# Kernel optimization log

Measured on AMD Instinct MI355X. Metric: run time of the kernel, lower is better.

Reference implementation:

```python
import jax, jax.numpy as jnp
import numpy as np

HEADS = 4
DIM_HEAD = 32
DIM = 128
HIDDEN = HEADS * DIM_HEAD  # 128


def setup_inputs() -> dict:
    key = jax.random.key(0)
    k1, k2, k3, k4 = jax.random.split(key, 4)
    B, C, H, W = 8, DIM, 128, 128
    x = jax.random.normal(k1, (B, C, H, W), dtype=jnp.float32)
    # 1x1 conv weights stored as [out_ch, in_ch] (kernel dims squeezed)
    w_qkv = jax.random.normal(k2, (3 * HIDDEN, DIM), dtype=jnp.float32) * (1.0 / np.sqrt(DIM))
    w_out = jax.random.normal(k3, (DIM, HIDDEN), dtype=jnp.float32) * (1.0 / np.sqrt(HIDDEN))
    b_out = jax.random.normal(k4, (DIM,), dtype=jnp.float32) * 0.01
    return {"x": x, "w_qkv": w_qkv, "w_out": w_out, "b_out": b_out}


def reference(x, w_qkv, w_out, b_out):
    b, c, h, w = x.shape
    n = h * w
    # 1x1 conv == per-pixel matmul over channels
    qkv = jnp.einsum('bchw,oc->bohw', x, w_qkv)            # [b, 3*HIDDEN, h, w]
    # channel layout: (qkv, heads, dim_head)
    qkv = qkv.reshape(b, 3, HEADS, DIM_HEAD, n)            # [b, 3, H, d, n]
    q, k, v = qkv[:, 0], qkv[:, 1], qkv[:, 2]
    k = jax.nn.softmax(k, axis=-1)                         # softmax over spatial n
    context = jnp.einsum('bhdn,bhen->bhde', k, v)          # [b, H, d, d] (tiny)
    out = jnp.einsum('bhde,bhdn->bhen', context, q)        # [b, H, d, n]
    out = out.reshape(b, HIDDEN, h, w)
    y = jnp.einsum('bchw,oc->bohw', out, w_out) + b_out[None, :, None, None]
    return y
```

## Files before the change

### kernel.cpp

```cpp
#include <hip/hip_runtime.h>
#include <math.h>

#define C_ 128
#define N_ 16384

#define WS_Z    0
#define WS_CTX  1024
#define WS_A    164864
#define WS_PCTX 295936
#define WS_PZ   (WS_PCTX + 512*4096)
#define WS_END  (WS_PZ + 512*128)

typedef __attribute__((ext_vector_type(8))) short bf16x8;
typedef __attribute__((ext_vector_type(4))) float f32x4;
typedef __attribute__((ext_vector_type(4))) unsigned int u32x4;
typedef __attribute__((ext_vector_type(2))) unsigned int u32x2;

__device__ __forceinline__ unsigned int pkbf(float a, float b) {
  unsigned int r;
  asm("v_cvt_pk_bf16_f32 %0, %1, %2" : "=v"(r) : "v"(a), "v"(b));
  return r;
}

__device__ __forceinline__ bf16x8 make_frag(float4 u, float4 v) {
  u32x4 q = {pkbf(u.x, u.y), pkbf(u.z, u.w), pkbf(v.x, v.y), pkbf(v.z, v.w)};
  return *(bf16x8*)&q;
}

__device__ __forceinline__ bf16x8 lds_frag16(const unsigned short* p) {
  u32x4 q = *(const u32x4*)p;
  return *(bf16x8*)&q;
}

__device__ __forceinline__ void load4(const float* p, float* o) {
  float4 v = *(const float4*)p;
  o[0] = v.x; o[1] = v.y; o[2] = v.z; o[3] = v.w;
}

__device__ __forceinline__ void* xsa(void* base, int row, int col_bytes) {
  return (void*)((char*)base + row * 272 + (col_bytes ^ (((row >> 4) & 3) << 4)));
}

template<bool ATOMIC>
__global__ __launch_bounds__(512, 2) void k1_kv_ctx(const float* __restrict__ x,
                                                    const float* __restrict__ wqkv,
                                                    float* __restrict__ ws) {
  __shared__ __attribute__((aligned(16))) unsigned short xs[64][136];
  __shared__ __attribute__((aligned(16))) unsigned short ekv[2][128][72];
  const int tid  = threadIdx.x;
  const int wave = tid >> 6;
  const int l15  = tid & 15;
  const int l4   = (tid >> 4) & 3;
  const int b    = blockIdx.y;
  const int j    = blockIdx.x;
  const int h    = wave & 3;
  const int t    = wave >> 2;
  const int kvrow0 = h * 32 + t * 128;
  const float* xb = x + (size_t)b * ((size_t)C_ * N_);

  const int sn4 = tid & 15;
  const int scq = tid >> 4;

  bf16x8 wf[2][4];
  #pragma unroll
  for (int mi = 0; mi < 2; ++mi)
    #pragma unroll
    for (int ki = 0; ki < 4; ++ki) {
      const float* p = wqkv + (size_t)(128 + kvrow0 + mi * 16 + l15) * C_ + ki * 32 + l4 * 8;
      wf[mi][ki] = make_frag(*(const float4*)p, *(const float4*)(p + 4));
    }

  {
    float va[4][4];
    #pragma unroll
    for (int r = 0; r < 4; ++r)
      load4(xb + (size_t)(scq * 4 + r) * N_ + j * 256 + sn4 * 4, va[r]);
    #pragma unroll
    for (int i = 0; i < 4; ++i) {
      u32x2 w = {pkbf(va[0][i], va[1][i]), pkbf(va[2][i], va[3][i])};
      *(u32x2*)xsa(xs, sn4 * 4 + i, scq * 8) = w;
    }
  }
  __syncthreads();

  const f32x4 z4 = {0.f, 0.f, 0.f, 0.f};
  f32x4 ctxacc[2][2];
  #pragma unroll
  for (int i = 0; i < 2; ++i)
    #pragma unroll
    for (int jj = 0; jj < 2; ++jj) ctxacc[i][jj] = z4;
  float zacc[2] = {0.f, 0.f};

  for (int st = 0; st < 4; ++st) {
    float pf[4][4];
    if (st < 3) {
      const int nbn = j * 256 + (st + 1) * 64;
      #pragma unroll
      for (int r = 0; r < 4; ++r)
        load4(xb + (size_t)(scq * 4 + r) * N_ + nbn + sn4 * 4, pf[r]);
    }

    #pragma unroll
    for (int half = 0; half < 2; ++half) {
      f32x4 acc[2][2];
      #pragma unroll
      for (int a = 0; a < 2; ++a)
        #pragma unroll
        for (int m = 0; m < 2; ++m) acc[a][m] = z4;
      #pragma unroll
      for (int ki = 0; ki < 4; ++ki) {
        bf16x8 bfr[2];
        #pragma unroll
        for (int ni2 = 0; ni2 < 2; ++ni2)
          bfr[ni2] = lds_frag16((const unsigned short*)
              xsa(xs, half * 32 + ni2 * 16 + l15, ki * 64 + l4 * 16));
        __builtin_amdgcn_s_setprio(1);
        #pragma unroll
        for (int ni2 = 0; ni2 < 2; ++ni2)
          #pragma unroll
          for (int mi = 0; mi < 2; ++mi)
            acc[ni2][mi] = __builtin_amdgcn_mfma_f32_16x16x32_bf16(
                bfr[ni2], wf[mi][ki], acc[ni2][mi], 0, 0, 0);
        __builtin_amdgcn_s_setprio(0);
      }
      #pragma unroll
      for (int ni2 = 0; ni2 < 2; ++ni2)
        #pragma unroll
        for (int mi = 0; mi < 2; ++mi) {
          float e0, e1, e2, e3;
          if (t == 0) {
            e0 = __expf(acc[ni2][mi][0]); e1 = __expf(acc[ni2][mi][1]);
            e2 = __expf(acc[ni2][mi][2]); e3 = __expf(acc[ni2][mi][3]);
            zacc[mi] += (e0 + e1) + (e2 + e3);
          } else {
            e0 = acc[ni2][mi][0]; e1 = acc[ni2][mi][1];
            e2 = acc[ni2][mi][2]; e3 = acc[ni2][mi][3];
          }
          u32x2 w = {pkbf(e0, e1), pkbf(e2, e3)};
          *(u32x2*)&ekv[t][h * 32 + mi * 16 + l15][(half * 2 + ni2) * 16 + l4 * 4] = w;
        }
    }
    __syncthreads();

    {
      bf16x8 af2[2], bv2[2];
      #pragma unroll
      for (int m2 = 0; m2 < 2; ++m2)
        af2[m2] = lds_frag16(&ekv[0][h * 32 + m2 * 16 + l15][t * 32 + l4 * 8]);
      #pragma unroll
      for (int n2 = 0; n2 < 2; ++n2)
        bv2[n2] = lds_frag16(&ekv[1][h * 32 + n2 * 16 + l15][t * 32 + l4 * 8]);
      __builtin_amdgcn_s_setprio(1);
      #pragma unroll
      for (int m2 = 0; m2 < 2; ++m2)
        #pragma unroll
        for (int n2 = 0; n2 < 2; ++n2)
          ctxacc[m2][n2] = __builtin_amdgcn_mfma_f32_16x16x32_bf16(
              af2[m2], bv2[n2], ctxacc[m2][n2], 0, 0, 0);
      __builtin_amdgcn_s_setprio(0);
    }

    if (st < 3) {
      #pragma unroll
      for (int i = 0; i < 4; ++i) {
        u32x2 w = {pkbf(pf[0][i], pf[1][i]), pkbf(pf[2][i], pf[3][i])};
        *(u32x2*)xsa(xs, sn4 * 4 + i, scq * 8) = w;
      }
    }
    __syncthreads();
  }

  {
    float* csh = (float*)ekv;
    if (t == 1) {
      #pragma unroll
      for (int m2 = 0; m2 < 2; ++m2)
        #pragma unroll
        for (int n2 = 0; n2 < 2; ++n2)
          #pragma unroll
          for (int r = 0; r < 4; ++r)
            csh[h * 1152 + (m2 * 16 + l4 * 4 + r) * 36 + n2 * 16 + l15] =
                ctxacc[m2][n2][r];
    }
    __syncthreads();
    if (t == 0) {
      #pragma unroll
      for (int m2 = 0; m2 < 2; ++m2)
        #pragma unroll
        for (int n2 = 0; n2 < 2; ++n2)
          #pragma unroll
          for (int r = 0; r < 4; ++r)
            ctxacc[m2][n2][r] +=
                csh[h * 1152 + (m2 * 16 + l4 * 4 + r) * 36 + n2 * 16 + l15];
      if (!ATOMIC) {
        float* ps = ws + WS_PCTX + (size_t)(b * 64 + j) * 4096 + h * 1024;
        #pragma unroll
        for (int m2 = 0; m2 < 2; ++m2)
          #pragma unroll
          for (int n2 = 0; n2 < 2; ++n2)
            #pragma unroll
            for (int r = 0; r < 4; ++r)
              ps[(m2 * 16 + l4 * 4 + r) * 32 + n2 * 16 + l15] = ctxacc[m2][n2][r];
      } else {
        float* ctx = ws + WS_CTX + (size_t)(b * 4 + h) * 1024;
        #pragma unroll
        for (int m2 = 0; m2 < 2; ++m2)
          #pragma unroll
          for (int n2 = 0; n2 < 2; ++n2)
            #pragma unroll
            for (int r = 0; r < 4; ++r)
              atomicAdd(&ctx[(m2 * 16 + l4 * 4 + r) * 32 + n2 * 16 + l15],
                        ctxacc[m2][n2][r]);
      }
      #pragma unroll
      for (int mi = 0; mi < 2; ++mi) {
        float z = zacc[mi];
        z += __shfl_xor(z, 16);
        z += __shfl_xor(z, 32);
        if ((tid & 48) == 0) {
          int row = h * 32 + mi * 16 + l15;
          if (!ATOMIC)
            ws[WS_PZ + (size_t)(b * 64 + j) * 128 + row] = z;
          else
            atomicAdd(&ws[WS_Z + b * 128 + row], z);
        }
      }
    }
  }
}

__global__ __launch_bounds__(256) void k1c(float* __restrict__ ws) {
  __shared__ float4 part[4][64];
  const int tid = threadIdx.x;
  const int eq = blockIdx.x;
  const int h  = blockIdx.y;
  const int b  = blockIdx.z;
  const int f4 = tid & 63;
  const int p  = tid >> 6;

  const float* base = ws + WS_PCTX + (size_t)(b * 64) * 4096
                         + h * 1024 + eq * 256 + f4 * 4;
  float4 s = {0.f, 0.f, 0.f, 0.f};
  #pragma unroll 8
  for (int q = 0; q < 16; ++q) {
    float4 v = *(const float4*)(base + (size_t)(p * 16 + q) * 4096);
    s.x += v.x; s.y += v.y; s.z += v.z; s.w += v.w;
  }
  part[p][f4] = s;

  if (eq == 0 && tid < 32) {
    const float* pz = ws + WS_PZ + (size_t)(b * 64) * 128 + h * 32 + tid;
    float z = 0.f;
    #pragma unroll 8
    for (int q = 0; q < 64; ++q) z += pz[(size_t)q * 128];
    ws[WS_Z + b * 128 + h * 32 + tid] = z;
  }
  __syncthreads();

  if (tid < 64) {
    float4 a = part[0][tid], c = part[1][tid], d = part[2][tid], e = part[3][tid];
    float4 o;
    o.x = (a.x + c.x) + (d.x + e.x);
    o.y = (a.y + c.y) + (d.y + e.y);
    o.z = (a.z + c.z) + (d.z + e.z);
    o.w = (a.w + c.w) + (d.w + e.w);
    *(float4*)(ws + WS_CTX + (size_t)(b * 4 + h) * 1024 + eq * 256 + tid * 4) = o;
  }
}

__global__ __launch_bounds__(256) void k2(const float* __restrict__ w_qkv,
                                          const float* __restrict__ w_out,
                                          float* __restrict__ ws) {
  __shared__ float bs[128][132];
  __shared__ float wqs[32][128];
  __shared__ float wos[32][132];
  __shared__ float cn[32][33];
  const int tid = threadIdx.x;
  const int oq = blockIdx.x, b = blockIdx.y;

  for (int h = 0; h < 4; ++h) {
    if (h) __syncthreads();
    const float* Z   = ws + WS_Z + b * 128 + h * 32;
    const float* ctx = ws + WS_CTX + ((b * 4 + h) * 32) * 32;
    #pragma unroll
    for (int k = 0; k < 4; ++k) {
      int idx = tid + k * 256;
      int d = idx >> 5, e = idx & 31;
      cn[d][e] = ctx[d * 32 + e] / Z[d];
    }
    #pragma unroll
    for (int k = 0; k < 4; ++k) {
      int idx = tid + k * 256;
      int d = idx >> 5, f4 = idx & 31;
      *(float4*)&wqs[d][f4 * 4] = *(const float4*)(w_qkv + (h * 32 + d) * 128 + f4 * 4);
    }
    __syncthreads();
    const int e = tid >> 3, cs = (tid & 7) * 16;
    float s[16];
    #pragma unroll
    for (int jj = 0; jj < 16; ++jj) s[jj] = 0.f;
    for (int d = 0; d < 32; ++d) {
      float v = cn[d][e];
      #pragma unroll
      for (int jj = 0; jj < 16; ++jj) s[jj] = fmaf(v, wqs[d][cs + jj], s[jj]);
    }
    #pragma unroll
    for (int jj = 0; jj < 16; ++jj) bs[h * 32 + e][cs + jj] = s[jj];
  }

  __syncthreads();
  #pragma unroll
  for (int k = 0; k < 4; ++k) {
    int idx = tid + k * 256;
    int r = idx >> 5, f4 = idx & 31;
    *(float4*)&wos[r][f4 * 4] = *(const float4*)(w_out + (oq * 32 + r) * 128 + f4 * 4);
  }
  __syncthreads();
  const int ol = tid >> 3, cq = (tid & 7) * 16;
  float s[16];
  #pragma unroll
  for (int jj = 0; jj < 16; ++jj) s[jj] = 0.f;
  for (int eg = 0; eg < 128; ++eg) {
    float w = wos[ol][eg];
    #pragma unroll
    for (int jj = 0; jj < 16; ++jj) s[jj] = fmaf(w, bs[eg][cq + jj], s[jj]);
  }
  float* A = ws + WS_A + ((size_t)b * 128 + oq * 32 + ol) * 128;
  #pragma unroll
  for (int jj = 0; jj < 16; ++jj) A[cq + jj] = s[jj];
}

__global__ __launch_bounds__(512, 2) void k3(const float* __restrict__ x,
                                             const float* __restrict__ bout,
                                             const float* __restrict__ ws,
                                             float* __restrict__ y) {
  __shared__ __attribute__((aligned(16))) unsigned short xs2[2][64][136];
  const int tid  = threadIdx.x;
  const int wave = tid >> 6;
  const int l15  = tid & 15;
  const int l4   = (tid >> 4) & 3;
  const int b    = blockIdx.y;
  const int n0   = blockIdx.x * 256;
  const float* xb = x + (size_t)b * ((size_t)C_ * N_);
  const float* A  = ws + WS_A + (size_t)b * 128 * 128;

  const int sn4 = tid & 15;
  const int scq = tid >> 4;

  bf16x8 af[4];
  #pragma unroll
  for (int ki = 0; ki < 4; ++ki) {
    const float* p = A + (size_t)(wave * 16 + l15) * 128 + ki * 32 + l4 * 8;
    af[ki] = make_frag(*(const float4*)p, *(const float4*)(p + 4));
  }
  const float bias = bout[wave * 16 + l15];

  {
    float va[4][4];
    #pragma unroll
    for (int r = 0; r < 4; ++r)
      load4(xb + (size_t)(scq * 4 + r) * N_ + n0 + sn4 * 4, va[r]);
    #pragma unroll
    for (int i = 0; i < 4; ++i) {
      u32x2 w = {pkbf(va[0][i], va[1][i]), pkbf(va[2][i], va[3][i])};
      *(u32x2*)xsa(&xs2[0][0][0], sn4 * 4 + i, scq * 8) = w;
    }
  }
  __syncthreads();

  const f32x4 z4 = {0.f, 0.f, 0.f, 0.f};
  float* yb = y + (size_t)b * ((size_t)128 * N_);

  for (int st = 0; st < 4; ++st) {
    const int nb = n0 + st * 64;

    float pf[4][4];
    if (st < 3) {
      #pragma unroll
      for (int r = 0; r < 4; ++r)
        load4(xb + (size_t)(scq * 4 + r) * N_ + nb + 64 + sn4 * 4, pf[r]);
    }

    f32x4 acc[4];
    #pragma unroll
    for (int ni = 0; ni < 4; ++ni) acc[ni] = z4;
    #pragma unroll
    for (int ki = 0; ki < 4; ++ki) {
      bf16x8 bfr[4];
      #pragma unroll
      for (int ni = 0; ni < 4; ++ni)
        bfr[ni] = lds_frag16((const unsigned short*)
            xsa(&xs2[st & 1][0][0], ni * 16 + l15, ki * 64 + l4 * 16));
      #pragma unroll
      for (int ni = 0; ni < 4; ++ni)
        acc[ni] = __builtin_amdgcn_mfma_f32_16x16x32_bf16(
            bfr[ni], af[ki], acc[ni], 0, 0, 0);
    }

    if (st < 3) {
      #pragma unroll
      for (int i = 0; i < 4; ++i) {
        u32x2 w = {pkbf(pf[0][i], pf[1][i]), pkbf(pf[2][i], pf[3][i])};
        *(u32x2*)xsa(&xs2[(st + 1) & 1][0][0], sn4 * 4 + i, scq * 8) = w;
      }
    }

    #pragma unroll
    for (int ni = 0; ni < 4; ++ni) {
      float4 o;
      o.x = acc[ni][0] + bias;
      o.y = acc[ni][1] + bias;
      o.z = acc[ni][2] + bias;
      o.w = acc[ni][3] + bias;
      *(float4*)(yb + (size_t)(wave * 16 + l15) * N_ + nb + ni * 16 + l4 * 4) = o;
    }

    if (st < 3) __syncthreads();
  }
}

extern "C" void kernel_launch(void* const* d_in, const int* in_sizes, int n_in,
                              void* d_out, int out_size, void* d_ws, size_t ws_size,
                              hipStream_t stream) {
  const float* x     = (const float*)d_in[0];
  const float* w_qkv = (const float*)d_in[1];
  const float* w_out = (const float*)d_in[2];
  const float* b_out = (const float*)d_in[3];
  float* y  = (float*)d_out;
  float* ws = (float*)d_ws;

  const bool partial = ws_size >= (size_t)WS_END * sizeof(float);
  if (partial) {
    k1_kv_ctx<false><<<dim3(64, 8), 512, 0, stream>>>(x, w_qkv, ws);
    k1c<<<dim3(4, 4, 8), 256, 0, stream>>>(ws);
  } else {
    hipMemsetAsync(ws, 0, (1024 + 32768) * sizeof(float), stream);
    k1_kv_ctx<true><<<dim3(64, 8), 512, 0, stream>>>(x, w_qkv, ws);
  }
  k2<<<dim3(4, 8), 256, 0, stream>>>(w_qkv, w_out, ws);
  k3<<<dim3(64, 8), 512, 0, stream>>>(x, b_out, ws, y);
}
```

Measured before the change: 73.16 us.

## Fuse all stages into one cooperative persistent kernel with grid syncs

Merges the context-projection, partial reduction, small weight-folding and output GEMM kernels into a single cooperative kernel of 512 blocks separated by grid-wide barriers, with a union of shared memory buffers per phase. The goal is to remove the launch gaps between the four kernels. The reduction and weight-folding stages are also redistributed across 512-thread blocks with a different loop split. The risks are the cost of three grid.sync barriers, the need for all 512 blocks to be co-resident (2 per CU), and higher register and LDS pressure from the union. A per-phase multi-launch fallback is kept for when cooperative launch is unavailable.

```diff
diff --git a/kernel.cpp b/kernel.cpp
--- a/kernel.cpp
+++ b/kernel.cpp
@@ -1,5 +1,8 @@
 #include <hip/hip_runtime.h>
+#include <hip/hip_cooperative_groups.h>
 #include <math.h>
+
+namespace cg = cooperative_groups;
 
 #define C_ 128
 #define N_ 16384
@@ -41,158 +44,168 @@
   return (void*)((char*)base + row * 272 + (col_bytes ^ (((row >> 4) & 3) << 4)));
 }
 
-template<bool ATOMIC>
-__global__ __launch_bounds__(512, 2) void k1_kv_ctx(const float* __restrict__ x,
-                                                    const float* __restrict__ wqkv,
-                                                    float* __restrict__ ws) {
-  __shared__ __attribute__((aligned(16))) unsigned short xs[64][136];
-  __shared__ __attribute__((aligned(16))) unsigned short ekv[2][128][72];
-  const int tid  = threadIdx.x;
-  const int wave = tid >> 6;
-  const int l15  = tid & 15;
-  const int l4   = (tid >> 4) & 3;
-  const int b    = blockIdx.y;
-  const int j    = blockIdx.x;
-  const int h    = wave & 3;
-  const int t    = wave >> 2;
-  const int kvrow0 = h * 32 + t * 128;
-  const float* xb = x + (size_t)b * ((size_t)C_ * N_);
-
-  const int sn4 = tid & 15;
-  const int scq = tid >> 4;
-
-  bf16x8 wf[2][4];
-  #pragma unroll
-  for (int mi = 0; mi < 2; ++mi)
-    #pragma unroll
-    for (int ki = 0; ki < 4; ++ki) {
-      const float* p = wqkv + (size_t)(128 + kvrow0 + mi * 16 + l15) * C_ + ki * 32 + l4 * 8;
-      wf[mi][ki] = make_frag(*(const float4*)p, *(const float4*)(p + 4));
-    }
-
-  {
-    float va[4][4];
-    #pragma unroll
-    for (int r = 0; r < 4; ++r)
-      load4(xb + (size_t)(scq * 4 + r) * N_ + j * 256 + sn4 * 4, va[r]);
-    #pragma unroll
-    for (int i = 0; i < 4; ++i) {
-      u32x2 w = {pkbf(va[0][i], va[1][i]), pkbf(va[2][i], va[3][i])};
-      *(u32x2*)xsa(xs, sn4 * 4 + i, scq * 8) = w;
-    }
-  }
-  __syncthreads();
-
-  const f32x4 z4 = {0.f, 0.f, 0.f, 0.f};
-  f32x4 ctxacc[2][2];
-  #pragma unroll
-  for (int i = 0; i < 2; ++i)
-    #pragma unroll
-    for (int jj = 0; jj < 2; ++jj) ctxacc[i][jj] = z4;
-  float zacc[2] = {0.f, 0.f};
-
-  for (int st = 0; st < 4; ++st) {
-    float pf[4][4];
-    if (st < 3) {
-      const int nbn = j * 256 + (st + 1) * 64;
+__global__ __launch_bounds__(512, 2) void fused(const float* __restrict__ x,
+                                                const float* __restrict__ wqkv,
+                                                const float* __restrict__ wout,
+                                                const float* __restrict__ bout,
+                                                float* __restrict__ ws,
+                                                float* __restrict__ y,
+                                                int phase) {
+  __shared__ __attribute__((aligned(16))) union {
+    struct { unsigned short xs[64][136]; unsigned short ekv[2][128][72]; } p1;
+    struct { float4 part[8][64]; } p2a;
+    struct { float cn[4][32][33]; float g[32][132]; float wst[32][132];
+             float zsh[128]; } p2b;
+    struct { unsigned short xs2[2][64][136]; } p3;
+  } sm;
+  const int tid = threadIdx.x;
+  const int bid = blockIdx.x;
+  cg::grid_group grid = cg::this_grid();
+
+  if (phase == 0 || phase == 1) {
+    const int j = bid & 63;
+    const int b = bid >> 6;
+    const int wave = tid >> 6;
+    const int l15  = tid & 15;
+    const int l4   = (tid >> 4) & 3;
+    const int h    = wave & 3;
+    const int t    = wave >> 2;
+    const int kvrow0 = h * 32 + t * 128;
+    const float* xb = x + (size_t)b * ((size_t)C_ * N_);
+    const int sn4 = tid & 15;
+    const int scq = tid >> 4;
+
+    bf16x8 wf[2][4];
+    #pragma unroll
+    for (int mi = 0; mi < 2; ++mi)
+      #pragma unroll
+      for (int ki = 0; ki < 4; ++ki) {
+        const float* p = wqkv + (size_t)(128 + kvrow0 + mi * 16 + l15) * C_ + ki * 32 + l4 * 8;
+        wf[mi][ki] = make_frag(*(const float4*)p, *(const float4*)(p + 4));
+      }
+
+    {
+      float va[4][4];
       #pragma unroll
       for (int r = 0; r < 4; ++r)
-        load4(xb + (size_t)(scq * 4 + r) * N_ + nbn + sn4 * 4, pf[r]);
-    }
-
-    #pragma unroll
-    for (int half = 0; half < 2; ++half) {
-      f32x4 acc[2][2];
-      #pragma unroll
-      for (int a = 0; a < 2; ++a)
-        #pragma unroll
-        for (int m = 0; m < 2; ++m) acc[a][m] = z4;
-      #pragma unroll
-      for (int ki = 0; ki < 4; ++ki) {
-        bf16x8 bfr[2];
+        load4(xb + (size_t)(scq * 4 + r) * N_ + j * 256 + sn4 * 4, va[r]);
+      #pragma unroll
+      for (int i = 0; i < 4; ++i) {
+        u32x2 w = {pkbf(va[0][i], va[1][i]), pkbf(va[2][i], va[3][i])};
+        *(u32x2*)xsa(&sm.p1.xs[0][0], sn4 * 4 + i, scq * 8) = w;
+      }
+    }
+    __syncthreads();
+
+    const f32x4 z4 = {0.f, 0.f, 0.f, 0.f};
+    f32x4 ctxacc[2][2];
+    #pragma unroll
+    for (int i = 0; i < 2; ++i)
+      #pragma unroll
+      for (int jj = 0; jj < 2; ++jj) ctxacc[i][jj] = z4;
+    float zacc[2] = {0.f, 0.f};
+
+    for (int st = 0; st < 4; ++st) {
+      float pf[4][4];
+      if (st < 3) {
+        const int nbn = j * 256 + (st + 1) * 64;
+        #pragma unroll
+        for (int r = 0; r < 4; ++r)
+          load4(xb + (size_t)(scq * 4 + r) * N_ + nbn + sn4 * 4, pf[r]);
+      }
+
+      #pragma unroll
+      for (int half = 0; half < 2; ++half) {
+        f32x4 acc[2][2];
+        #pragma unroll
+        for (int a = 0; a < 2; ++a)
+          #pragma unroll
+          for (int m = 0; m < 2; ++m) acc[a][m] = z4;
+        #pragma unroll
+        for (int ki = 0; ki < 4; ++ki) {
+          bf16x8 bfr[2];
+          #pragma unroll
+          for (int ni2 = 0; ni2 < 2; ++ni2)
+            bfr[ni2] = lds_frag16((const unsigned short*)
+                xsa(&sm.p1.xs[0][0], half * 32 + ni2 * 16 + l15, ki * 64 + l4 * 16));
+          __builtin_amdgcn_s_setprio(1);
+          #pragma unroll
+          for (int ni2 = 0; ni2 < 2; ++ni2)
+            #pragma unroll
+            for (int mi = 0; mi < 2; ++mi)
+              acc[ni2][mi] = __builtin_amdgcn_mfma_f32_16x16x32_bf16(
+                  bfr[ni2], wf[mi][ki], acc[ni2][mi], 0, 0, 0);
+          __builtin_amdgcn_s_setprio(0);
+        }
         #pragma unroll
         for (int ni2 = 0; ni2 < 2; ++ni2)
-          bfr[ni2] = lds_frag16((const unsigned short*)
-              xsa(xs, half * 32 + ni2 * 16 + l15, ki * 64 + l4 * 16));
+          #pragma unroll
+          for (int mi = 0; mi < 2; ++mi) {
+            float e0, e1, e2, e3;
+            if (t == 0) {
+              e0 = __expf(acc[ni2][mi][0]); e1 = __expf(acc[ni2][mi][1]);
+              e2 = __expf(acc[ni2][mi][2]); e3 = __expf(acc[ni2][mi][3]);
+              zacc[mi] += (e0 + e1) + (e2 + e3);
+            } else {
+              e0 = acc[ni2][mi][0]; e1 = acc[ni2][mi][1];
+              e2 = acc[ni2][mi][2]; e3 = acc[ni2][mi][3];
+            }
+            u32x2 w = {pkbf(e0, e1), pkbf(e2, e3)};
+            *(u32x2*)&sm.p1.ekv[t][h * 32 + mi * 16 + l15][(half * 2 + ni2) * 16 + l4 * 4] = w;
+          }
+      }
+      __syncthreads();
+
+      {
+        bf16x8 af2[2], bv2[2];
+        #pragma unroll
+        for (int m2 = 0; m2 < 2; ++m2)
+          af2[m2] = lds_frag16(&sm.p1.ekv[0][h * 32 + m2 * 16 + l15][t * 32 + l4 * 8]);
+        #pragma unroll
+        for (int n2 = 0; n2 < 2; ++n2)
+          bv2[n2] = lds_frag16(&sm.p1.ekv[1][h * 32 + n2 * 16 + l15][t * 32 + l4 * 8]);
         __builtin_amdgcn_s_setprio(1);
         #pragma unroll
-        for (int ni2 = 0; ni2 < 2; ++ni2)
-          #pragma unroll
-          for (int mi = 0; mi < 2; ++mi)
-            acc[ni2][mi] = __builtin_amdgcn_mfma_f32_16x16x32_bf16(
-                bfr[ni2], wf[mi][ki], acc[ni2][mi], 0, 0, 0);
+        for (int m2 = 0; m2 < 2; ++m2)
+          #pragma unroll
+          for (int n2 = 0; n2 < 2; ++n2)
+            ctxacc[m2][n2] = __builtin_amdgcn_mfma_f32_16x16x32_bf16(
+                af2[m2], bv2[n2], ctxacc[m2][n2], 0, 0, 0);
         __builtin_amdgcn_s_setprio(0);
       }
-      #pragma unroll
-      for (int ni2 = 0; ni2 < 2; ++ni2)
-        #pragma unroll
-        for (int mi = 0; mi < 2; ++mi) {
-          float e0, e1, e2, e3;
-          if (t == 0) {
-            e0 = __expf(acc[ni2][mi][0]); e1 = __expf(acc[ni2][mi][1]);
-            e2 = __expf(acc[ni2][mi][2]); e3 = __expf(acc[ni2][mi][3]);
-            zacc[mi] += (e0 + e1) + (e2 + e3);
-          } else {
-            e0 = acc[ni2][mi][0]; e1 = acc[ni2][mi][1];
-            e2 = acc[ni2][mi][2]; e3 = acc[ni2][mi][3];
-          }
-          u32x2 w = {pkbf(e0, e1), pkbf(e2, e3)};
-          *(u32x2*)&ekv[t][h * 32 + mi * 16 + l15][(half * 2 + ni2) * 16 + l4 * 4] = w;
+
+      if (st < 3) {
+        #pragma unroll
+        for (int i = 0; i < 4; ++i) {
+          u32x2 w = {pkbf(pf[0][i], pf[1][i]), pkbf(pf[2][i], pf[3][i])};
+          *(u32x2*)xsa(&sm.p1.xs[0][0], sn4 * 4 + i, scq * 8) = w;
         }
-    }
-    __syncthreads();
+      }
+      __syncthreads();
+    }
 
     {
-      bf16x8 af2[2], bv2[2];
-      #pragma unroll
-      for (int m2 = 0; m2 < 2; ++m2)
-        af2[m2] = lds_frag16(&ekv[0][h * 32 + m2 * 16 + l15][t * 32 + l4 * 8]);
-      #pragma unroll
-      for (int n2 = 0; n2 < 2; ++n2)
-        bv2[n2] = lds_frag16(&ekv[1][h * 32 + n2 * 16 + l15][t * 32 + l4 * 8]);
-      __builtin_amdgcn_s_setprio(1);
-      #pragma unroll
-      for (int m2 = 0; m2 < 2; ++m2)
-        #pragma unroll
-        for (int n2 = 0; n2 < 2; ++n2)
-          ctxacc[m2][n2] = __builtin_amdgcn_mfma_f32_16x16x32_bf16(
-              af2[m2], bv2[n2], ctxacc[m2][n2], 0, 0, 0);
-      __builtin_amdgcn_s_setprio(0);
-    }
-
-    if (st < 3) {
-      #pragma unroll
-      for (int i = 0; i < 4; ++i) {
-        u32x2 w = {pkbf(pf[0][i], pf[1][i]), pkbf(pf[2][i], pf[3][i])};
-        *(u32x2*)xsa(xs, sn4 * 4 + i, scq * 8) = w;
-      }
-    }
-    __syncthreads();
-  }
-
-  {
-    float* csh = (float*)ekv;
-    if (t == 1) {
-      #pragma unroll
-      for (int m2 = 0; m2 < 2; ++m2)
-        #pragma unroll
-        for (int n2 = 0; n2 < 2; ++n2)
-          #pragma unroll
-          for (int r = 0; r < 4; ++r)
-            csh[h * 1152 + (m2 * 16 + l4 * 4 + r) * 36 + n2 * 16 + l15] =
-                ctxacc[m2][n2][r];
-    }
-    __syncthreads();
-    if (t == 0) {
-      #pragma unroll
-      for (int m2 = 0; m2 < 2; ++m2)
-        #pragma unroll
-        for (int n2 = 0; n2 < 2; ++n2)
-          #pragma unroll
-          for (int r = 0; r < 4; ++r)
-            ctxacc[m2][n2][r] +=
-                csh[h * 1152 + (m2 * 16 + l4 * 4 + r) * 36 + n2 * 16 + l15];
-      if (!ATOMIC) {
+      float* csh = (float*)&sm.p1.ekv[0][0][0];
+      if (t == 1) {
+        #pragma unroll
+        for (int m2 = 0; m2 < 2; ++m2)
+          #pragma unroll
+          for (int n2 = 0; n2 < 2; ++n2)
+            #pragma unroll
+            for (int r = 0; r < 4; ++r)
+              csh[h * 1152 + (m2 * 16 + l4 * 4 + r) * 36 + n2 * 16 + l15] =
+                  ctxacc[m2][n2][r];
+      }
+      __syncthreads();
+      if (t == 0) {
+        #pragma unroll
+        for (int m2 = 0; m2 < 2; ++m2)
+          #pragma unroll
+          for (int n2 = 0; n2 < 2; ++n2)
+            #pragma unroll
+            for (int r = 0; r < 4; ++r)
+              ctxacc[m2][n2][r] +=
+                  csh[h * 1152 + (m2 * 16 + l4 * 4 + r) * 36 + n2 * 16 + l15];
         float* ps = ws + WS_PCTX + (size_t)(b * 64 + j) * 4096 + h * 1024;
         #pragma unroll
         for (int m2 = 0; m2 < 2; ++m2)
@@ -201,221 +214,184 @@
             #pragma unroll
             for (int r = 0; r < 4; ++r)
               ps[(m2 * 16 + l4 * 4 + r) * 32 + n2 * 16 + l15] = ctxacc[m2][n2][r];
-      } else {
-        float* ctx = ws + WS_CTX + (size_t)(b * 4 + h) * 1024;
-        #pragma unroll
-        for (int m2 = 0; m2 < 2; ++m2)
-          #pragma unroll
-          for (int n2 = 0; n2 < 2; ++n2)
-            #pragma unroll
-            for (int r = 0; r < 4; ++r)
-              atomicAdd(&ctx[(m2 * 16 + l4 * 4 + r) * 32 + n2 * 16 + l15],
-                        ctxacc[m2][n2][r]);
-      }
-      #pragma unroll
-      for (int mi = 0; mi < 2; ++mi) {
-        float z = zacc[mi];
-        z += __shfl_xor(z, 16);
-        z += __shfl_xor(z, 32);
-        if ((tid & 48) == 0) {
-          int row = h * 32 + mi * 16 + l15;
-          if (!ATOMIC)
-            ws[WS_PZ + (size_t)(b * 64 + j) * 128 + row] = z;
-          else
-            atomicAdd(&ws[WS_Z + b * 128 + row], z);
+        #pragma unroll
+        for (int mi = 0; mi < 2; ++mi) {
+          float z = zacc[mi];
+          z += __shfl_xor(z, 16);
+          z += __shfl_xor(z, 32);
+          if ((tid & 48) == 0)
+            ws[WS_PZ + (size_t)(b * 64 + j) * 128 + h * 32 + mi * 16 + l15] = z;
         }
       }
     }
   }
-}
-
-__global__ __launch_bounds__(256) void k1c(float* __restrict__ ws) {
-  __shared__ float4 part[4][64];
-  const int tid = threadIdx.x;
-  const int eq = blockIdx.x;
-  const int h  = blockIdx.y;
-  const int b  = blockIdx.z;
-  const int f4 = tid & 63;
-  const int p  = tid >> 6;
-
-  const float* base = ws + WS_PCTX + (size_t)(b * 64) * 4096
-                         + h * 1024 + eq * 256 + f4 * 4;
-  float4 s = {0.f, 0.f, 0.f, 0.f};
-  #pragma unroll 8
-  for (int q = 0; q < 16; ++q) {
-    float4 v = *(const float4*)(base + (size_t)(p * 16 + q) * 4096);
-    s.x += v.x; s.y += v.y; s.z += v.z; s.w += v.w;
+  if (phase == 0) grid.sync();
+
+  if ((phase == 0 || phase == 2) && bid < 128) {
+    const int eq = bid & 3, h = (bid >> 2) & 3, b = bid >> 4;
+    const int f4 = tid & 63, p = tid >> 6;
+    const float* base = ws + WS_PCTX + (size_t)(b * 64) * 4096
+                           + h * 1024 + eq * 256 + f4 * 4;
+    float4 s = {0.f, 0.f, 0.f, 0.f};
+    #pragma unroll
+    for (int q = 0; q < 8; ++q) {
+      float4 v = *(const float4*)(base + (size_t)(p * 8 + q) * 4096);
+      s.x += v.x; s.y += v.y; s.z += v.z; s.w += v.w;
+    }
+    sm.p2a.part[p][f4] = s;
+    if (eq == 0 && tid < 32) {
+      const float* pz = ws + WS_PZ + (size_t)(b * 64) * 128 + h * 32 + tid;
+      float z = 0.f;
+      #pragma unroll 8
+      for (int q = 0; q < 64; ++q) z += pz[(size_t)q * 128];
+      ws[WS_Z + b * 128 + h * 32 + tid] = z;
+    }
+    __syncthreads();
+    if (tid < 64) {
+      float4 o = {0.f, 0.f, 0.f, 0.f};
+      #pragma unroll
+      for (int p2 = 0; p2 < 8; ++p2) {
+        float4 a = sm.p2a.part[p2][tid];
+        o.x += a.x; o.y += a.y; o.z += a.z; o.w += a.w;
+      }
+      *(float4*)(ws + WS_CTX + (size_t)(b * 4 + h) * 1024 + eq * 256 + tid * 4) = o;
+    }
   }
-  part[p][f4] = s;
-
-  if (eq == 0 && tid < 32) {
-    const float* pz = ws + WS_PZ + (size_t)(b * 64) * 128 + h * 32 + tid;
-    float z = 0.f;
-    #pragma unroll 8
-    for (int q = 0; q < 64; ++q) z += pz[(size_t)q * 128];
-    ws[WS_Z + b * 128 + h * 32 + tid] = z;
+  if (phase == 0) grid.sync();
+
+  if ((phase == 0 || phase == 3) && bid < 32) {
+    const int oq = bid & 3, b = bid >> 2;
+    if (tid < 128) sm.p2b.zsh[tid] = ws[WS_Z + b * 128 + tid];
+    __syncthreads();
+    {
+      const int idx = tid * 8;
+      const int h = idx >> 10, d = (idx >> 5) & 31, e0 = idx & 31;
+      const float zi = 1.f / sm.p2b.zsh[h * 32 + d];
+      const float* p = ws + WS_CTX + (size_t)b * 4096 + idx;
+      #pragma unroll
+      for (int i = 0; i < 8; ++i) sm.p2b.cn[h][d][e0 + i] = p[i] * zi;
+    }
+    {
+      const int r = tid >> 4, f = (tid & 15) * 8;
+      *(float4*)&sm.p2b.wst[r][f]     = *(const float4*)(wout + (oq * 32 + r) * 128 + f);
+      *(float4*)&sm.p2b.wst[r][f + 4] = *(const float4*)(wout + (oq * 32 + r) * 128 + f + 4);
+    }
+    __syncthreads();
+    const int o = tid >> 4, q8 = (tid & 15) * 8;
+    float gacc[8];
+    #pragma unroll
+    for (int i = 0; i < 8; ++i) {
+      const int hd = q8 + i, h = hd >> 5, d = hd & 31;
+      float s = 0.f;
+      for (int e = 0; e < 32; ++e)
+        s = fmaf(sm.p2b.wst[o][h * 32 + e], sm.p2b.cn[h][d][e], s);
+      gacc[i] = s;
+    }
+    #pragma unroll
+    for (int i = 0; i < 8; ++i) sm.p2b.g[o][q8 + i] = gacc[i];
+    float s3[8];
+    #pragma unroll
+    for (int jj = 0; jj < 8; ++jj) s3[jj] = 0.f;
+    for (int h = 0; h < 4; ++h) {
+      __syncthreads();
+      const int r = tid >> 4, f = (tid & 15) * 8;
+      *(float4*)&sm.p2b.wst[r][f]     = *(const float4*)(wqkv + (h * 32 + r) * 128 + f);
+      *(float4*)&sm.p2b.wst[r][f + 4] = *(const float4*)(wqkv + (h * 32 + r) * 128 + f + 4);
+      __syncthreads();
+      for (int d = 0; d < 32; ++d) {
+        const float gg = sm.p2b.g[o][h * 32 + d];
+        #pragma unroll
+        for (int jj = 0; jj < 8; ++jj)
+          s3[jj] = fmaf(gg, sm.p2b.wst[d][q8 + jj], s3[jj]);
+      }
+    }
+    float* A = ws + WS_A + ((size_t)b * 128 + oq * 32 + o) * 128;
+    #pragma unroll
+    for (int jj = 0; jj < 8; ++jj) A[q8 + jj] = s3[jj];
   }
-  __syncthreads();
-
-  if (tid < 64) {
-    float4 a = part[0][tid], c = part[1][tid], d = part[2][tid], e = part[3][tid];
-    float4 o;
-    o.x = (a.x + c.x) + (d.x + e.x);
-    o.y = (a.y + c.y) + (d.y + e.y);
-    o.z = (a.z + c.z) + (d.z + e.z);
-    o.w = (a.w + c.w) + (d.w + e.w);
-    *(float4*)(ws + WS_CTX + (size_t)(b * 4 + h) * 1024 + eq * 256 + tid * 4) = o;
-  }
-}
-
-__global__ __launch_bounds__(256) void k2(const float* __restrict__ w_qkv,
-                                          const float* __restrict__ w_out,
-                                          float* __restrict__ ws) {
-  __shared__ float bs[128][132];
-  __shared__ float wqs[32][128];
-  __shared__ float wos[32][132];
-  __shared__ float cn[32][33];
-  const int tid = threadIdx.x;
-  const int oq = blockIdx.x, b = blockIdx.y;
-
-  for (int h = 0; h < 4; ++h) {
-    if (h) __syncthreads();
-    const float* Z   = ws + WS_Z + b * 128 + h * 32;
-    const float* ctx = ws + WS_CTX + ((b * 4 + h) * 32) * 32;
-    #pragma unroll
-    for (int k = 0; k < 4; ++k) {
-      int idx = tid + k * 256;
-      int d = idx >> 5, e = idx & 31;
-      cn[d][e] = ctx[d * 32 + e] / Z[d];
-    }
-    #pragma unroll
-    for (int k = 0; k < 4; ++k) {
-      int idx = tid + k * 256;
-      int d = idx >> 5, f4 = idx & 31;
-      *(float4*)&wqs[d][f4 * 4] = *(const float4*)(w_qkv + (h * 32 + d) * 128 + f4 * 4);
+  if (phase == 0) grid.sync();
+
+  if (phase == 0 || phase == 4) {
+    const int j = bid & 63;
+    const int b = bid >> 6;
+    const int wave = tid >> 6;
+    const int l15  = tid & 15;
+    const int l4   = (tid >> 4) & 3;
+    const int n0   = j * 256;
+    const float* xb = x + (size_t)b * ((size_t)C_ * N_);
+    const float* A  = ws + WS_A + (size_t)b * 128 * 128;
+    const int sn4 = tid & 15;
+    const int scq = tid >> 4;
+
+    bf16x8 af[4];
+    #pragma unroll
+    for (int ki = 0; ki < 4; ++ki) {
+      const float* p = A + (size_t)(wave * 16 + l15) * 128 + ki * 32 + l4 * 8;
+      af[ki] = make_frag(*(const float4*)p, *(const float4*)(p + 4));
+    }
+    const float bias = bout[wave * 16 + l15];
+
+    {
+      float va[4][4];
+      #pragma unroll
+      for (int r = 0; r < 4; ++r)
+        load4(xb + (size_t)(scq * 4 + r) * N_ + n0 + sn4 * 4, va[r]);
+      #pragma unroll
+      for (int i = 0; i < 4; ++i) {
+        u32x2 w = {pkbf(va[0][i], va[1][i]), pkbf(va[2][i], va[3][i])};
+        *(u32x2*)xsa(&sm.p3.xs2[0][0][0], sn4 * 4 + i, scq * 8) = w;
+      }
     }
     __syncthreads();
-    const int e = tid >> 3, cs = (tid & 7) * 16;
-    float s[16];
-    #pragma unroll
-    for (int jj = 0; jj < 16; ++jj) s[jj] = 0.f;
-    for (int d = 0; d < 32; ++d) {
-      float v = cn[d][e];
-      #pragma unroll
-      for (int jj = 0; jj < 16; ++jj) s[jj] = fmaf(v, wqs[d][cs + jj], s[jj]);
-    }
-    #pragma unroll
-    for (int jj = 0; jj < 16; ++jj) bs[h * 32 + e][cs + jj] = s[jj];
-  }
-
-  __syncthreads();
-  #pragma unroll
-  for (int k = 0; k < 4; ++k) {
-    int idx = tid + k * 256;
-    int r = idx >> 5, f4 = idx & 31;
-    *(float4*)&wos[r][f4 * 4] = *(const float4*)(w_out + (oq * 32 + r) * 128 + f4 * 4);
-  }
-  __syncthreads();
-  const int ol = tid >> 3, cq = (tid & 7) * 16;
-  float s[16];
-  #pragma unroll
-  for (int jj = 0; jj < 16; ++jj) s[jj] = 0.f;
-  for (int eg = 0; eg < 128; ++eg) {
-    float w = wos[ol][eg];
-    #pragma unroll
-    for (int jj = 0; jj < 16; ++jj) s[jj] = fmaf(w, bs[eg][cq + jj], s[jj]);
-  }
-  float* A = ws + WS_A + ((size_t)b * 128 + oq * 32 + ol) * 128;
-  #pragma unroll
-  for (int jj = 0; jj < 16; ++jj) A[cq + jj] = s[jj];
-}
-
-__global__ __launch_bounds__(512, 2) void k3(const float* __restrict__ x,
-                                             const float* __restrict__ bout,
-                                             const float* __restrict__ ws,
-                                             float* __restrict__ y) {
-  __shared__ __attribute__((aligned(16))) unsigned short xs2[2][64][136];
-  const int tid  = threadIdx.x;
-  const int wave = tid >> 6;
-  const int l15  = tid & 15;
-  const int l4   = (tid >> 4) & 3;
-  const int b    = blockIdx.y;
-  const int n0   = blockIdx.x * 256;
-  const float* xb = x + (size_t)b * ((size_t)C_ * N_);
-  const float* A  = ws + WS_A + (size_t)b * 128 * 128;
-
-  const int sn4 = tid & 15;
-  const int scq = tid >> 4;
-
-  bf16x8 af[4];
-  #pragma unroll
-  for (int ki = 0; ki < 4; ++ki) {
-    const float* p = A + (size_t)(wave * 16 + l15) * 128 + ki * 32 + l4 * 8;
-    af[ki] = make_frag(*(const float4*)p, *(const float4*)(p + 4));
-  }
-  const float bias = bout[wave * 16 + l15];
-
-  {
-    float va[4][4];
-    #pragma unroll
-    for (int r = 0; r < 4; ++r)
-      load4(xb + (size_t)(scq * 4 + r) * N_ + n0 + sn4 * 4, va[r]);
-    #pragma unroll
-    for (int i = 0; i < 4; ++i) {
-      u32x2 w = {pkbf(va[0][i], va[1][i]), pkbf(va[2][i], va[3][i])};
-      *(u32x2*)xsa(&xs2[0][0][0], sn4 * 4 + i, scq * 8) = w;
-    }
-  }
-  __syncthreads();
-
-  const f32x4 z4 = {0.f, 0.f, 0.f, 0.f};
-  float* yb = y + (size_t)b * ((size_t)128 * N_);
-
-  for (int st = 0; st < 4; ++st) {
-    const int nb = n0 + st * 64;
-
-    float pf[4][4];
-    if (st < 3) {
-      #pragma unroll
-      for (int r = 0; r < 4; ++r)
-        load4(xb + (size_t)(scq * 4 + r) * N_ + nb + 64 + sn4 * 4, pf[r]);
-    }
-
-    f32x4 acc[4];
-    #pragma unroll
-    for (int ni = 0; ni < 4; ++ni) acc[ni] = z4;
-    #pragma unroll
-    for (int ki = 0; ki < 4; ++ki) {
-      bf16x8 bfr[4];
-      #pragma unroll
-      for (int ni = 0; ni < 4; ++ni)
-        bfr[ni] = lds_frag16((const unsigned short*)
-            xsa(&xs2[st & 1][0][0], ni * 16 + l15, ki * 64 + l4 * 16));
-      #pragma unroll
-      for (int ni = 0; ni < 4; ++ni)
-        acc[ni] = __builtin_amdgcn_mfma_f32_16x16x32_bf16(
-            bfr[ni], af[ki], acc[ni], 0, 0, 0);
-    }
-
-    if (st < 3) {
-      #pragma unroll
-      for (int i = 0; i < 4; ++i) {
-        u32x2 w = {pkbf(pf[0][i], pf[1][i]), pkbf(pf[2][i], pf[3][i])};
-        *(u32x2*)xsa(&xs2[(st + 1) & 1][0][0], sn4 * 4 + i, scq * 8) = w;
-      }
-    }
-
-    #pragma unroll
-    for (int ni = 0; ni < 4; ++ni) {
-      float4 o;
-      o.x = acc[ni][0] + bias;
-      o.y = acc[ni][1] + bias;
-      o.z = acc[ni][2] + bias;
-      o.w = acc[ni][3] + bias;
-      *(float4*)(yb + (size_t)(wave * 16 + l15) * N_ + nb + ni * 16 + l4 * 4) = o;
-    }
-
-    if (st < 3) __syncthreads();
+
+    const f32x4 z4 = {0.f, 0.f, 0.f, 0.f};
+    float* yb = y + (size_t)b * ((size_t)128 * N_);
+
+    for (int st = 0; st < 4; ++st) {
+      const int nb = n0 + st * 64;
+      float pf[4][4];
+      if (st < 3) {
+        #pragma unroll
+        for (int r = 0; r < 4; ++r)
+          load4(xb + (size_t)(scq * 4 + r) * N_ + nb + 64 + sn4 * 4, pf[r]);
+      }
+
+      f32x4 acc[4];
+      #pragma unroll
+      for (int ni = 0; ni < 4; ++ni) acc[ni] = z4;
+      #pragma unroll
+      for (int ki = 0; ki < 4; ++ki) {
+        bf16x8 bfr[4];
+        #pragma unroll
+        for (int ni = 0; ni < 4; ++ni)
+          bfr[ni] = lds_frag16((const unsigned short*)
+              xsa(&sm.p3.xs2[st & 1][0][0], ni * 16 + l15, ki * 64 + l4 * 16));
+        #pragma unroll
+        for (int ni = 0; ni < 4; ++ni)
+          acc[ni] = __builtin_amdgcn_mfma_f32_16x16x32_bf16(
+              bfr[ni], af[ki], acc[ni], 0, 0, 0);
+      }
+
+      if (st < 3) {
+        #pragma unroll
+        for (int i = 0; i < 4; ++i) {
+          u32x2 w = {pkbf(pf[0][i], pf[1][i]), pkbf(pf[2][i], pf[3][i])};
+          *(u32x2*)xsa(&sm.p3.xs2[(st + 1) & 1][0][0], sn4 * 4 + i, scq * 8) = w;
+        }
+      }
+
+      #pragma unroll
+      for (int ni = 0; ni < 4; ++ni) {
+        float4 o;
+        o.x = acc[ni][0] + bias;
+        o.y = acc[ni][1] + bias;
+        o.z = acc[ni][2] + bias;
+        o.w = acc[ni][3] + bias;
+        *(float4*)(yb + (size_t)(wave * 16 + l15) * N_ + nb + ni * 16 + l4 * 4) = o;
+      }
+
+      if (st < 3) __syncthreads();
+    }
   }
 }
 
@@ -429,14 +405,21 @@
   float* y  = (float*)d_out;
   float* ws = (float*)d_ws;
 
-  const bool partial = ws_size >= (size_t)WS_END * sizeof(float);
-  if (partial) {
-    k1_kv_ctx<false><<<dim3(64, 8), 512, 0, stream>>>(x, w_qkv, ws);
-    k1c<<<dim3(4, 4, 8), 256, 0, stream>>>(ws);
-  } else {
-    hipMemsetAsync(ws, 0, (1024 + 32768) * sizeof(float), stream);
-    k1_kv_ctx<true><<<dim3(64, 8), 512, 0, stream>>>(x, w_qkv, ws);
+  int maxb = 0;
+  hipError_t oe = hipOccupancyMaxActiveBlocksPerMultiprocessor(&maxb, fused, 512, 0);
+  const bool coop = (oe == hipSuccess && maxb >= 2 &&
+                     ws_size >= (size_t)WS_END * sizeof(float));
+
+  if (coop) {
+    int ph = 0;
+    void* args[] = {(void*)&x, (void*)&w_qkv, (void*)&w_out, (void*)&b_out,
+                    (void*)&ws, (void*)&y, (void*)&ph};
+    hipError_t e = hipLaunchCooperativeKernel(reinterpret_cast<void*>(fused),
+                                              dim3(512), dim3(512), args, 0, stream);
+    if (e == hipSuccess) return;
   }
-  k2<<<dim3(4, 8), 256, 0, stream>>>(w_qkv, w_out, ws);
-  k3<<<dim3(64, 8), 512, 0, stream>>>(x, b_out, ws, y);
-}
+  fused<<<512, 512, 0, stream>>>(x, w_qkv, w_out, b_out, ws, y, 1);
+  fused<<<128, 512, 0, stream>>>(x, w_qkv, w_out, b_out, ws, y, 2);
+  fused<<< 32, 512, 0, stream>>>(x, w_qkv, w_out, b_out, ws, y, 3);
+  fused<<<512, 512, 0, stream>>>(x, w_qkv, w_out, b_out, ws, y, 4);
+}
```

After: 71.87 us. No clear change (-1.8%).
